# Kernel optimization log

Measured on AMD Instinct MI355X. Metric: run time of the kernel, lower is better.

## Reference

```python
import jax, jax.numpy as jnp
import numpy as np

N, E, F_IN, H, K = 50000, 800000, 64, 128, 4


def setup_inputs() -> dict:
    key = jax.random.key(0)
    k0, k1, k2, k3 = jax.random.split(key, 4)
    features = jax.random.normal(k0, (N, F_IN), dtype=jnp.float32)
    edge_index = jax.random.randint(k1, (2, E), 0, N, dtype=jnp.int32)
    # ChebConv parameters: one [F_IN, H] weight per Chebyshev order + shared bias
    cheb_w = jax.random.normal(k2, (K, F_IN, H), dtype=jnp.float32) * 0.05
    cheb_b = jnp.zeros((H,), dtype=jnp.float32)
    # final Linear(H, 1)
    final_w = jax.random.normal(k3, (H, 1), dtype=jnp.float32) * 0.05
    final_b = jnp.zeros((1,), dtype=jnp.float32)
    return dict(features=features, edge_index=edge_index, cheb_w=cheb_w,
                cheb_b=cheb_b, final_w=final_w, final_b=final_b)


def _cheb_conv(x, edge_index, w, b):
    # PyG ChebConv, sym normalization, lambda_max = 2.0, no self-loops in input:
    # L_hat = (2/lambda_max) * (I - D^-1/2 A D^-1/2) - I = -D^-1/2 A D^-1/2
    row, col = edge_index[0], edge_index[1]
    n = x.shape[0]
    deg = jax.ops.segment_sum(jnp.ones((row.shape[0],), dtype=x.dtype), row,
                              num_segments=n)
    dinv = jnp.where(deg > 0, jax.lax.rsqrt(jnp.maximum(deg, 1e-12)), 0.0)
    ew = -dinv[row] * dinv[col]  # [E] normalized (negated) edge weights

    def spmm(z):  # L_hat @ z via gather-multiply-scatter
        return jax.ops.segment_sum(z[col] * ew[:, None], row, num_segments=n)

    Tx0 = x
    out = Tx0 @ w[0]
    Tx1 = spmm(Tx0)
    if w.shape[0] > 1:
        out = out + Tx1 @ w[1]
    for k in range(2, w.shape[0]):  # Chebyshev recursion T_k = 2 L T_{k-1} - T_{k-2}
        Tx2 = 2.0 * spmm(Tx1) - Tx0
        out = out + Tx2 @ w[k]
        Tx0, Tx1 = Tx1, Tx2
    return out + b


def reference(features, edge_index, cheb_w, cheb_b, final_w, final_b):
    h = jnp.tanh(_cheb_conv(features, edge_index, cheb_w, cheb_b))  # [N, H]
    return (h @ final_w + final_b).reshape(-1)  # [N]
```

## Files before the change

### kernel.cpp

```cpp
#include <hip/hip_runtime.h>
#include <hip/hip_fp16.h>
#include <math.h>


#define FIN 64
#define HDIM 128

typedef _Float16 half8 __attribute__((ext_vector_type(8)));
typedef float f32x4 __attribute__((ext_vector_type(4)));

union U16 { uint4 u; __half2 h2[4]; half8 h8; };

__global__ void fused_pre(const int* __restrict__ row, int* __restrict__ deg, int E,
                          const float4* __restrict__ fsrc, uint4* __restrict__ fdst, int n8,
                          const float* __restrict__ W, uint4* __restrict__ bfrag) {
    int i = blockIdx.x * blockDim.x + threadIdx.x;
    if (i < E) atomicAdd(&deg[row[i]], 1);
    if (i < n8) {
        float4 a = fsrc[i * 2], b = fsrc[i * 2 + 1];
        U16 v;
        v.h2[0] = __float22half2_rn(make_float2(a.x, a.y));
        v.h2[1] = __float22half2_rn(make_float2(a.z, a.w));
        v.h2[2] = __float22half2_rn(make_float2(b.x, b.y));
        v.h2[3] = __float22half2_rn(make_float2(b.z, b.w));
        fdst[i] = v.u;
    }
    if (i < 8 * 8 * 64) {
        int lane = i & 63;
        int ht = (i >> 6) & 7;
        int kk = i >> 9;
        int h = ht * 16 + (lane & 15);
        int kb = kk * 32 + (lane >> 4) * 8;
        U16 v;
#pragma unroll
        for (int j = 0; j < 4; ++j) {
            float a = W[(kb + 2 * j) * HDIM + h];
            float b = W[(kb + 2 * j + 1) * HDIM + h];
            v.h2[j] = __float22half2_rn(make_float2(a, b));
        }
        bfrag[i] = v.u;
    }
}

__global__ void alloc_rows(const int* __restrict__ deg, float* __restrict__ dinv,
                           int2* __restrict__ rowspan, int* __restrict__ cursor,
                           int* __restrict__ ctr, int n, int stride8) {
    int i = blockIdx.x * blockDim.x + threadIdx.x;
    int lane = threadIdx.x & 63;
    int d = (i < n) ? deg[i] : 0;
    if (i < n) dinv[i] = (d > 0) ? rsqrtf((float)d) : 0.f;
    int pd = (i < n) ? ((d + 3) & ~3) : 0;
    int x = pd;
    for (int off = 1; off < 64; off <<= 1) {
        int t = __shfl_up(x, off, 64);
        if (lane >= off) x += t;
    }
    int excl = x - pd;
    int total = __shfl(x, 63, 64);
    int base = 0;
    if (lane == 0 && total > 0) base = atomicAdd(ctr, total);
    base = __shfl(base, 0, 64);
    if (i < n) {
        int b = base + excl;
        rowspan[i] = make_int2(b, b + pd);
        cursor[(i & 7) * stride8 + (i >> 3)] = b;
    }
}

__global__ void scatter_xcd(const int* __restrict__ row, const int* __restrict__ col,
                            const float* __restrict__ dinv, int* __restrict__ cursor,
                            int2* __restrict__ epk, int E, int stride8) {
    int xcd = blockIdx.x & 7;
    int e = (blockIdx.x >> 3) * blockDim.x + threadIdx.x;
    if (e < E) {
        int r = row[e];
        if ((r & 7) == xcd) {
            int c = col[e];
            int p = atomicAdd(&cursor[xcd * stride8 + (r >> 3)], 1);
            float w = -dinv[r] * dinv[c];
            epk[p] = make_int2(c, __float_as_int(w));
        }
    }
}

__global__ __launch_bounds__(256) void spmm_h(
        const int2* __restrict__ rowspan, const int2* __restrict__ epk,
        const uint4* __restrict__ in8, const uint4* __restrict__ prev8,
        float scale, uint4* __restrict__ out8, int n) {
    int lane = threadIdx.x & 63;
    int wid = (blockIdx.x * blockDim.x + threadIdx.x) >> 6;
    int li = lane & 7, g = lane >> 3;
    int r = wid * 8 + g;
    if (r >= n) return;
    int2 span = rowspan[r];
    int s = span.x, e = span.y;

    U16 pv;
    if (prev8) pv.u = prev8[(size_t)r * 8 + li];

    float acc[8];
#pragma unroll
    for (int j = 0; j < 8; ++j) acc[j] = 0.f;

    if (s < e) {
        int2 mc[4], mn[4];
        U16 vc[4];
#pragma unroll
        for (int j = 0; j < 4; ++j) mc[j] = epk[s + j];
#pragma unroll
        for (int j = 0; j < 4; ++j) vc[j].u = in8[(size_t)mc[j].x * 8 + li];
        if (s + 4 < e) {
#pragma unroll
            for (int j = 0; j < 4; ++j) mn[j] = epk[s + 4 + j];
        }
        for (int p = s;;) {
            bool more = p + 4 < e;
            bool more2 = p + 8 < e;
            U16 vn[4];
            int2 m2[4];
            if (more) {
#pragma unroll
                for (int j = 0; j < 4; ++j) vn[j].u = in8[(size_t)mn[j].x * 8 + li];
            }
            if (more2) {
#pragma unroll
                for (int j = 0; j < 4; ++j) m2[j] = epk[p + 8 + j];
            }
            float w0 = __int_as_float(mc[0].y), w1 = __int_as_float(mc[1].y);
            float w2 = __int_as_float(mc[2].y), w3 = __int_as_float(mc[3].y);
#pragma unroll
            for (int j = 0; j < 4; ++j) {
                float2 f0 = __half22float2(vc[0].h2[j]);
                float2 f1 = __half22float2(vc[1].h2[j]);
                float2 f2 = __half22float2(vc[2].h2[j]);
                float2 f3 = __half22float2(vc[3].h2[j]);
                acc[2 * j]     = fmaf(w0, f0.x, acc[2 * j]);
                acc[2 * j + 1] = fmaf(w0, f0.y, acc[2 * j + 1]);
                acc[2 * j]     = fmaf(w1, f1.x, acc[2 * j]);
                acc[2 * j + 1] = fmaf(w1, f1.y, acc[2 * j + 1]);
                acc[2 * j]     = fmaf(w2, f2.x, acc[2 * j]);
                acc[2 * j + 1] = fmaf(w2, f2.y, acc[2 * j + 1]);
                acc[2 * j]     = fmaf(w3, f3.x, acc[2 * j]);
                acc[2 * j + 1] = fmaf(w3, f3.y, acc[2 * j + 1]);
            }
            if (!more) break;
#pragma unroll
            for (int j = 0; j < 4; ++j) {
                mc[j] = mn[j];
                mn[j] = m2[j];
                vc[j] = vn[j];
            }
            p += 4;
        }
    }

    float res[8];
    if (prev8) {
#pragma unroll
        for (int t = 0; t < 4; ++t) {
            float2 f = __half22float2(pv.h2[t]);
            res[2 * t]     = fmaf(scale, acc[2 * t], -f.x);
            res[2 * t + 1] = fmaf(scale, acc[2 * t + 1], -f.y);
        }
    } else {
#pragma unroll
        for (int j = 0; j < 8; ++j) res[j] = scale * acc[j];
    }
    U16 ru;
#pragma unroll
    for (int t = 0; t < 4; ++t)
        ru.h2[t] = __float22half2_rn(make_float2(res[2 * t], res[2 * t + 1]));
    out8[(size_t)r * 8 + li] = ru.u;
}

__device__ inline float tanh_fast(float x) {
    x = fmaxf(-10.f, fminf(10.f, x));
    float e = __expf(2.f * x);
    return (e - 1.f) / (e + 1.f);
}

__global__ __launch_bounds__(256) void gemm_mfma(
        const uint4* __restrict__ tx0, const uint4* __restrict__ tx1,
        const uint4* __restrict__ tx2, const uint4* __restrict__ tx3,
        const uint4* __restrict__ bfrag,
        const float* __restrict__ cheb_b, const float* __restrict__ fw,
        const float* __restrict__ fb, float* __restrict__ out, int n) {
    int tid = threadIdx.x;
    int lane = tid & 63;
    int wave = tid >> 6;
    int q = lane >> 4, m = lane & 15;
    int node_base = blockIdx.x * 64 + wave * 16;
    int node = node_base + m;
    size_t nd = (node < n) ? (size_t)node : 0;

    f32x4 acc[8];
#pragma unroll
    for (int t = 0; t < 8; ++t) acc[t] = (f32x4){0.f, 0.f, 0.f, 0.f};

    const uint4* txs[4] = {tx0, tx1, tx2, tx3};
#pragma unroll
    for (int kk = 0; kk < 8; ++kk) {
        U16 av;
        av.u = txs[kk >> 1][nd * 8 + (kk & 1) * 4 + q];
#pragma unroll
        for (int ht = 0; ht < 8; ++ht) {
            U16 bv;
            bv.u = bfrag[(kk * 8 + ht) * 64 + lane];
            acc[ht] = __builtin_amdgcn_mfma_f32_16x16x32_f16(av.h8, bv.h8, acc[ht], 0, 0, 0);
        }
    }

    float s[4] = {0.f, 0.f, 0.f, 0.f};
#pragma unroll
    for (int ht = 0; ht < 8; ++ht) {
        int h = ht * 16 + m;
        float cb = cheb_b[h];
        float fv = fw[h];
#pragma unroll
        for (int r = 0; r < 4; ++r)
            s[r] = fmaf(tanh_fast(acc[ht][r] + cb), fv, s[r]);
    }
#pragma unroll
    for (int r = 0; r < 4; ++r) {
        for (int msk = 1; msk < 16; msk <<= 1)
            s[r] += __shfl_xor(s[r], msk, 64);
    }
    if (m == 0) {
        float fb0 = fb[0];
#pragma unroll
        for (int r = 0; r < 4; ++r) {
            int o = node_base + q * 4 + r;
            if (o < n) out[o] = s[r] + fb0;
        }
    }
}

extern "C" void kernel_launch(void* const* d_in, const int* in_sizes, int n_in,
                              void* d_out, int out_size, void* d_ws, size_t ws_size,
                              hipStream_t stream) {
    const float* features = (const float*)d_in[0];
    const int*   edge_index = (const int*)d_in[1];
    const float* cheb_w  = (const float*)d_in[2];
    const float* cheb_b  = (const float*)d_in[3];
    const float* final_w = (const float*)d_in[4];
    const float* final_b = (const float*)d_in[5];
    int N = in_sizes[0] / FIN;
    int E = in_sizes[1] / 2;
    const int* row = edge_index;
    const int* col = edge_index + E;
    int E_pad = E + 4 * N;
    int stride8 = (N + 7) / 8;

    char* p = (char*)d_ws;
    auto alloc = [&](size_t bytes) {
        char* r = p;
        p += (bytes + 255) & ~(size_t)255;
        return r;
    };
    int*   ctr    = (int*)alloc(256);
    int*   deg    = (int*)alloc((size_t)N * 4);
    int2*  epk    = (int2*)alloc((size_t)E_pad * 8);
    size_t zero_bytes = (char*)(epk + E_pad) - (char*)ctr;
    float* dinv   = (float*)alloc((size_t)N * 4);
    int2*  rowspan= (int2*)alloc((size_t)N * 8);
    int*   cursor = (int*)alloc((size_t)(stride8 * 8) * 4);
    uint4* feath  = (uint4*)alloc((size_t)N * FIN * 2);
    uint4* tx1h   = (uint4*)alloc((size_t)N * FIN * 2);
    uint4* tx2h   = (uint4*)alloc((size_t)N * FIN * 2);
    uint4* tx3h   = (uint4*)alloc((size_t)N * FIN * 2);
    uint4* bfrag  = (uint4*)alloc(4096 * 16);

    hipMemsetAsync(ctr, 0, zero_bytes, stream);
    int n8 = N * FIN / 8;
    int eb = (E + 255) / 256;
    fused_pre<<<eb, 256, 0, stream>>>(row, deg, E, (const float4*)features, feath,
                                      n8, cheb_w, bfrag);
    alloc_rows<<<(N + 255) / 256, 256, 0, stream>>>(deg, dinv, rowspan, cursor,
                                                    ctr, N, stride8);
    scatter_xcd<<<eb * 8, 256, 0, stream>>>(row, col, dinv, cursor, epk, E, stride8);

    int spmm_blocks = (((N + 7) / 8) * 64 + 255) / 256;
    spmm_h<<<spmm_blocks, 256, 0, stream>>>(rowspan, epk, feath, nullptr, 1.f, tx1h, N);
    spmm_h<<<spmm_blocks, 256, 0, stream>>>(rowspan, epk, tx1h, feath, 2.f, tx2h, N);
    spmm_h<<<spmm_blocks, 256, 0, stream>>>(rowspan, epk, tx2h, tx1h, 2.f, tx3h, N);

    gemm_mfma<<<(N + 63) / 64, 256, 0, stream>>>(feath, tx1h, tx2h, tx3h, bfrag,
                                                 cheb_b, final_w, final_b,
                                                 (float*)d_out, N);
}
```

Before: 216.9 us.

## Bin rows by degree and process SpMM rows in degree-sorted order

Adds a counting sort of rows into 32 degree bins (histogram in alloc_rows, a scan kernel, and a sort_rows kernel that writes a row permutation). The SpMM kernels then process rows through this rowlist, so the 8 rows handled by one wavefront have similar degrees and lanes idle less on divergent loop lengths. The cost is two extra kernel launches, ballot loops over 32 bins, and one more indirection in SpMM. Row order inside a bin is nondeterministic, and outputs and prev reads become scattered rather than contiguous.

After: 314.4 us. 44.9% more time.

```diff
diff --git a/kernel.cpp b/kernel.cpp
--- a/kernel.cpp
+++ b/kernel.cpp
@@ -42,9 +42,12 @@
     }
 }
 
+__device__ inline int deg_bin(int pd) { return min(pd >> 2, 31); }
+
 __global__ void alloc_rows(const int* __restrict__ deg, float* __restrict__ dinv,
                            int2* __restrict__ rowspan, int* __restrict__ cursor,
-                           int* __restrict__ ctr, int n, int stride8) {
+                           int* __restrict__ ctr, int* __restrict__ binCount,
+                           int n, int stride8) {
     int i = blockIdx.x * blockDim.x + threadIdx.x;
     int lane = threadIdx.x & 63;
     int d = (i < n) ? deg[i] : 0;
@@ -64,6 +67,42 @@
         int b = base + excl;
         rowspan[i] = make_int2(b, b + pd);
         cursor[(i & 7) * stride8 + (i >> 3)] = b;
+    }
+    int mybin = (i < n) ? deg_bin(pd) : -1;
+    for (int b = 0; b < 32; ++b) {
+        unsigned long long mask = __ballot(mybin == b);
+        if (mask && lane == (__ffsll((long long)mask) - 1))
+            atomicAdd(&binCount[b], __popcll(mask));
+    }
+}
+
+__global__ void bin_scan(const int* __restrict__ binCount, int* __restrict__ binCursor) {
+    int lane = threadIdx.x;
+    int c = (lane < 32) ? binCount[lane] : 0;
+    int x = c;
+    for (int off = 1; off < 64; off <<= 1) {
+        int t = __shfl_up(x, off, 64);
+        if (lane >= off) x += t;
+    }
+    if (lane < 32) binCursor[lane] = x - c;
+}
+
+__global__ void sort_rows(const int* __restrict__ deg, int* __restrict__ binCursor,
+                          int* __restrict__ rowlist, int n) {
+    int i = blockIdx.x * blockDim.x + threadIdx.x;
+    int lane = threadIdx.x & 63;
+    int pd = (i < n) ? ((deg[i] + 3) & ~3) : 0;
+    int mybin = (i < n) ? deg_bin(pd) : -1;
+    for (int b = 0; b < 32; ++b) {
+        unsigned long long mask = __ballot(mybin == b);
+        if (mybin == b) {
+            int leader = __ffsll((long long)mask) - 1;
+            int base = 0;
+            if (lane == leader) base = atomicAdd(&binCursor[b], __popcll(mask));
+            base = __shfl(base, leader, 64);
+            int posin = __popcll(mask & ((1ull << lane) - 1ull));
+            rowlist[base + posin] = i;
+        }
     }
 }
 
@@ -84,14 +123,16 @@
 }
 
 __global__ __launch_bounds__(256) void spmm_h(
-        const int2* __restrict__ rowspan, const int2* __restrict__ epk,
-        const uint4* __restrict__ in8, const uint4* __restrict__ prev8,
-        float scale, uint4* __restrict__ out8, int n) {
+        const int* __restrict__ rowlist, const int2* __restrict__ rowspan,
+        const int2* __restrict__ epk, const uint4* __restrict__ in8,
+        const uint4* __restrict__ prev8, float scale,
+        uint4* __restrict__ out8, int n) {
     int lane = threadIdx.x & 63;
     int wid = (blockIdx.x * blockDim.x + threadIdx.x) >> 6;
     int li = lane & 7, g = lane >> 3;
-    int r = wid * 8 + g;
-    if (r >= n) return;
+    int idx = wid * 8 + g;
+    if (idx >= n) return;
+    int r = rowlist[idx];
     int2 span = rowspan[r];
     int s = span.x, e = span.y;
 
@@ -257,18 +298,21 @@
         p += (bytes + 255) & ~(size_t)255;
         return r;
     };
-    int*   ctr    = (int*)alloc(256);
-    int*   deg    = (int*)alloc((size_t)N * 4);
-    int2*  epk    = (int2*)alloc((size_t)E_pad * 8);
+    int*   ctr     = (int*)alloc(256);
+    int*   binCount= (int*)alloc(32 * 4);
+    int*   deg     = (int*)alloc((size_t)N * 4);
+    int2*  epk     = (int2*)alloc((size_t)E_pad * 8);
     size_t zero_bytes = (char*)(epk + E_pad) - (char*)ctr;
-    float* dinv   = (float*)alloc((size_t)N * 4);
-    int2*  rowspan= (int2*)alloc((size_t)N * 8);
-    int*   cursor = (int*)alloc((size_t)(stride8 * 8) * 4);
-    uint4* feath  = (uint4*)alloc((size_t)N * FIN * 2);
-    uint4* tx1h   = (uint4*)alloc((size_t)N * FIN * 2);
-    uint4* tx2h   = (uint4*)alloc((size_t)N * FIN * 2);
-    uint4* tx3h   = (uint4*)alloc((size_t)N * FIN * 2);
-    uint4* bfrag  = (uint4*)alloc(4096 * 16);
+    float* dinv    = (float*)alloc((size_t)N * 4);
+    int2*  rowspan = (int2*)alloc((size_t)N * 8);
+    int*   cursor  = (int*)alloc((size_t)(stride8 * 8) * 4);
+    int*   binCursor = (int*)alloc(32 * 4);
+    int*   rowlist = (int*)alloc((size_t)N * 4);
+    uint4* feath   = (uint4*)alloc((size_t)N * FIN * 2);
+    uint4* tx1h    = (uint4*)alloc((size_t)N * FIN * 2);
+    uint4* tx2h    = (uint4*)alloc((size_t)N * FIN * 2);
+    uint4* tx3h    = (uint4*)alloc((size_t)N * FIN * 2);
+    uint4* bfrag   = (uint4*)alloc(4096 * 16);
 
     hipMemsetAsync(ctr, 0, zero_bytes, stream);
     int n8 = N * FIN / 8;
@@ -276,13 +320,18 @@
     fused_pre<<<eb, 256, 0, stream>>>(row, deg, E, (const float4*)features, feath,
                                       n8, cheb_w, bfrag);
     alloc_rows<<<(N + 255) / 256, 256, 0, stream>>>(deg, dinv, rowspan, cursor,
-                                                    ctr, N, stride8);
+                                                    ctr, binCount, N, stride8);
+    bin_scan<<<1, 64, 0, stream>>>(binCount, binCursor);
+    sort_rows<<<(N + 255) / 256, 256, 0, stream>>>(deg, binCursor, rowlist, N);
     scatter_xcd<<<eb * 8, 256, 0, stream>>>(row, col, dinv, cursor, epk, E, stride8);
 
     int spmm_blocks = (((N + 7) / 8) * 64 + 255) / 256;
-    spmm_h<<<spmm_blocks, 256, 0, stream>>>(rowspan, epk, feath, nullptr, 1.f, tx1h, N);
-    spmm_h<<<spmm_blocks, 256, 0, stream>>>(rowspan, epk, tx1h, feath, 2.f, tx2h, N);
-    spmm_h<<<spmm_blocks, 256, 0, stream>>>(rowspan, epk, tx2h, tx1h, 2.f, tx3h, N);
+    spmm_h<<<spmm_blocks, 256, 0, stream>>>(rowlist, rowspan, epk, feath, nullptr,
+                                            1.f, tx1h, N);
+    spmm_h<<<spmm_blocks, 256, 0, stream>>>(rowlist, rowspan, epk, tx1h, feath,
+                                            2.f, tx2h, N);
+    spmm_h<<<spmm_blocks, 256, 0, stream>>>(rowlist, rowspan, epk, tx2h, tx1h,
+                                            2.f, tx3h, N);
 
     gemm_mfma<<<(N + 63) / 64, 256, 0, stream>>>(feath, tx1h, tx2h, tx3h, bfrag,
                                                  cheb_b, final_w, final_b,
```
